# Performance work log

Hardware: AMD Instinct MI355X
Metric: run time of the kernel (lower is better)

## Reference

```python
import jax, jax.numpy as jnp
import numpy as np

N_BATCH, S, CH = 16384, 7, 30  # B*5+num_classes = 2*5+20
CO_COORD, CO_NOOBJ = 5.0, 0.5


def setup_inputs() -> dict:
    key = jax.random.key(0)
    k1, k2, k3 = jax.random.split(key, 3)
    preds = jax.random.uniform(k1, (N_BATCH, S, S, CH), dtype=jnp.float32)
    targets = jax.random.uniform(k2, (N_BATCH, S, S, CH), dtype=jnp.float32)
    obj = (jax.random.uniform(k3, (N_BATCH, S, S)) > 0.7).astype(jnp.float32)
    targets = targets.at[..., 4].set(obj * targets[..., 4] + obj * 1e-3)
    return {"preds": preds, "targets": targets}


def reference(preds, targets):
    # NOTE: faithful to the original torch code, including its bug where
    # coo_target is taken from preds (so box_target/class_target == the
    # predictions), making loc_loss and class_loss identically zero while
    # contain_loss compares pred confidence against (detached) IoU.
    N = preds.shape[0]
    P = preds.reshape(-1, CH)            # [NC, 30], NC = N*S*S
    T = targets.reshape(-1, CH)
    conf_t = T[:, 4]
    coo = (conf_t > 0).astype(preds.dtype)   # cells with object
    noo = (conf_t == 0).astype(preds.dtype)  # cells without object

    # --- no-object confidence loss (channels 4 and 9) ---
    nooobj_loss = jnp.sum(noo * ((P[:, 4] - T[:, 4]) ** 2 + (P[:, 9] - T[:, 9]) ** 2))

    # --- per-cell box matching (vectorized version of the python loop) ---
    boxes = P[:, :10].reshape(-1, 2, 5)       # [NC, 2, 5] predicted boxes
    xy = boxes[..., :2] / 14.0                # 14.0 == 2*S hardcoded upstream
    wh = boxes[..., 2:4]
    lt1 = xy - 0.5 * wh                       # [NC, 2, 2]
    rb1 = xy + 0.5 * wh
    tbox = boxes[:, 0]                        # box2 = box_target[i] == first pred box (bug)
    lt2 = tbox[:, :2] / 14.0 - 0.5 * tbox[:, 2:4]  # [NC, 2]
    rb2 = tbox[:, :2] / 14.0 + 0.5 * tbox[:, 2:4]

    ilt = jnp.maximum(lt1, lt2[:, None, :])
    irb = jnp.minimum(rb1, rb2[:, None, :])
    iwh = jnp.maximum(irb - ilt, 0.0)
    inter = iwh[..., 0] * iwh[..., 1]                    # [NC, 2]
    area1 = (rb1 - lt1)[..., 0] * (rb1 - lt1)[..., 1]    # [NC, 2]
    area2 = ((rb2 - lt2)[..., 0] * (rb2 - lt2)[..., 1])[:, None]
    iou = inter / (area1 + area2 - inter)                # [NC, 2]

    max_iou = jnp.max(iou, axis=1)                       # [NC]
    idx = jnp.argmax(iou, axis=1)                        # [NC] in {0,1}
    resp = jnp.take_along_axis(boxes, idx[:, None, None], axis=1)[:, 0]       # responsible box
    nresp = jnp.take_along_axis(boxes, (1 - idx)[:, None, None], axis=1)[:, 0]
    tgt_resp = resp  # box_target == box_pred due to the upstream bug

    # contain: pred conf vs detached IoU (original uses max_iou.data)
    contain_loss = jnp.sum(coo * (resp[:, 4] - jax.lax.stop_gradient(max_iou)) ** 2)
    # loc: identically zero given the bug, but computed faithfully
    loc_loss = (jnp.sum(coo[:, None] * (resp[:, :2] - tgt_resp[:, :2]) ** 2)
                + jnp.sum(coo[:, None] * (jnp.sqrt(resp[:, 2:4]) - jnp.sqrt(tgt_resp[:, 2:4])) ** 2))
    # not-responsible box: target conf zeroed
    not_contain_loss = jnp.sum(coo * nresp[:, 4] ** 2)
    # class loss: class_target also taken from preds (bug) -> zero
    cls = P[:, 10:]
    class_loss = jnp.sum(coo[:, None] * (cls - cls) ** 2)

    total = (CO_COORD * loc_loss + contain_loss + CO_NOOBJ * not_contain_loss
             + CO_NOOBJ * nooobj_loss + class_loss) / N
    return total
```

## Files before the change

### kernel.cpp

```cpp
#include <hip/hip_runtime.h>


#define TILE 256

__device__ __forceinline__ float cell_loss(const float p[10], float t4, float t9) {
    float coo = (t4 > 0.0f) ? 1.0f : 0.0f;
    float noo = (t4 == 0.0f) ? 1.0f : 0.0f;

    float d4 = p[4] - t4;
    float d9 = p[9] - t9;
    float noo_term = noo * (d4 * d4 + d9 * d9);

    float lt2x = p[0] / 14.0f - 0.5f * p[2];
    float lt2y = p[1] / 14.0f - 0.5f * p[3];
    float rb2x = p[0] / 14.0f + 0.5f * p[2];
    float rb2y = p[1] / 14.0f + 0.5f * p[3];
    float area2 = (rb2x - lt2x) * (rb2y - lt2y);

    float iou[2];
    #pragma unroll
    for (int b = 0; b < 2; ++b) {
        float x = p[5 * b] / 14.0f;
        float y = p[5 * b + 1] / 14.0f;
        float w = p[5 * b + 2];
        float h = p[5 * b + 3];
        float lt1x = x - 0.5f * w, lt1y = y - 0.5f * h;
        float rb1x = x + 0.5f * w, rb1y = y + 0.5f * h;
        float iltx = fmaxf(lt1x, lt2x), ilty = fmaxf(lt1y, lt2y);
        float irbx = fminf(rb1x, rb2x), irby = fminf(rb1y, rb2y);
        float iwx = fmaxf(irbx - iltx, 0.0f);
        float iwy = fmaxf(irby - ilty, 0.0f);
        float inter = iwx * iwy;
        float area1 = (rb1x - lt1x) * (rb1y - lt1y);
        iou[b] = inter / (area1 + area2 - inter);
    }

    int idx;
    float max_iou;
    if (isnan(iou[0]))      { idx = 0; max_iou = iou[0]; }
    else if (isnan(iou[1])) { idx = 1; max_iou = iou[1]; }
    else                    { idx = (iou[1] > iou[0]) ? 1 : 0;
                              max_iou = fmaxf(iou[0], iou[1]); }

    float resp4  = p[5 * idx + 4];
    float nresp4 = p[5 * (1 - idx) + 4];
    float cdiff  = resp4 - max_iou;
    return coo * (cdiff * cdiff + 0.5f * nresp4 * nresp4) + 0.5f * noo_term;
}

__global__ __launch_bounds__(256) void yolo_loss_kernel(
    const float* __restrict__ preds,
    const float* __restrict__ targets,
    float* __restrict__ partials,
    int ncells)
{
    __shared__ float4 smem4[768];
    __shared__ float  warp_sums[4];
    float2* S2 = reinterpret_cast<float2*>(smem4);
    float*  Tc = reinterpret_cast<float*>(smem4 + 640);

    const int tid = threadIdx.x;
    const long tile0 = (long)blockIdx.x * TILE;
    float contrib = 0.0f;

    if (tile0 + TILE <= ncells) {
        const float4* gp = reinterpret_cast<const float4*>(preds + tile0 * 30);
        const float4* gt = reinterpret_cast<const float4*>(targets + tile0 * 30);

        float4 pv[3];
        #pragma unroll
        for (int k = 0; k < 3; ++k) {
            int L = tid + 256 * k;
            int pair = L / 6, rr = L - pair * 6;
            int r = (rr < 3) ? rr : rr + 4;
            pv[k] = gp[pair * 15 + r];
        }
        float4 tv[2];
        #pragma unroll
        for (int k = 0; k < 2; ++k) {
            int L = tid + 256 * k;
            int pair = L / 4, rr = L & 3;
            int r = (rr < 2) ? rr + 1 : rr + 6;
            tv[k] = gt[pair * 15 + r];
        }

        #pragma unroll
        for (int k = 0; k < 3; ++k) {
            int L = tid + 256 * k;
            int pair = L / 6, rr = L - pair * 6;
            if (rr == 2) {
                S2[(pair * 5 + 2) * 2] = make_float2(pv[k].x, pv[k].y);
            } else if (rr == 3) {
                S2[(pair * 5 + 2) * 2 + 1] = make_float2(pv[k].z, pv[k].w);
            } else {
                int slot = (rr < 2) ? rr : rr - 1;
                smem4[pair * 5 + slot] = pv[k];
            }
        }
        #pragma unroll
        for (int k = 0; k < 2; ++k) {
            int L = tid + 256 * k;
            int pair = L / 4, rr = L & 3;
            float v = (rr == 0) ? tv[k].x : (rr == 1) ? tv[k].y
                    : (rr == 2) ? tv[k].z : tv[k].w;
            Tc[pair * 4 + rr] = v;
        }
        __syncthreads();

        float p[10];
        #pragma unroll
        for (int k = 0; k < 5; ++k) {
            float2 q = S2[5 * tid + k];
            p[2 * k]     = q.x;
            p[2 * k + 1] = q.y;
        }
        float t4 = Tc[2 * tid];
        float t9 = Tc[2 * tid + 1];
        contrib = cell_loss(p, t4, t9);
    } else {
        long cell = tile0 + tid;
        if (cell < ncells) {
            long base = cell * 30;
            float p[10];
            #pragma unroll
            for (int k = 0; k < 5; ++k) {
                float2 v = *reinterpret_cast<const float2*>(preds + base + 2 * k);
                p[2 * k] = v.x;
                p[2 * k + 1] = v.y;
            }
            contrib = cell_loss(p, targets[base + 4], targets[base + 9]);
        }
        __syncthreads();
    }

    #pragma unroll
    for (int off = 32; off > 0; off >>= 1)
        contrib += __shfl_down(contrib, off, 64);

    int lane = tid & 63;
    int wid  = tid >> 6;
    if (lane == 0) warp_sums[wid] = contrib;
    __syncthreads();

    if (tid == 0) {
        partials[blockIdx.x] = warp_sums[0] + warp_sums[1] + warp_sums[2] + warp_sums[3];
    }
}

__global__ __launch_bounds__(256) void yolo_reduce_kernel(
    const float* __restrict__ partials,
    float* __restrict__ out,
    int nparts)
{
    __shared__ float warp_sums[4];
    const int tid = threadIdx.x;

    float s = 0.0f;
    for (int i = tid; i < nparts; i += 256)
        s += partials[i];

    #pragma unroll
    for (int off = 32; off > 0; off >>= 1)
        s += __shfl_down(s, off, 64);

    int lane = tid & 63;
    int wid  = tid >> 6;
    if (lane == 0) warp_sums[wid] = s;
    __syncthreads();

    if (tid == 0) {
        out[0] = (warp_sums[0] + warp_sums[1] + warp_sums[2] + warp_sums[3])
                 * (1.0f / 16384.0f);
    }
}

extern "C" void kernel_launch(void* const* d_in, const int* in_sizes, int n_in,
                              void* d_out, int out_size, void* d_ws, size_t ws_size,
                              hipStream_t stream) {
    const float* preds   = (const float*)d_in[0];
    const float* targets = (const float*)d_in[1];
    float* out = (float*)d_out;
    float* partials = (float*)d_ws;

    int ncells = in_sizes[0] / 30;
    int grid = (ncells + TILE - 1) / TILE;

    yolo_loss_kernel<<<grid, 256, 0, stream>>>(preds, targets, partials, ncells);
    yolo_reduce_kernel<<<1, 256, 0, stream>>>(partials, out, grid);
}
```

Measured before the change: 37.25 us.

## Process two tiles per block, prefetching the second tile during compute of the first

```diff
diff --git a/kernel.cpp b/kernel.cpp
--- a/kernel.cpp
+++ b/kernel.cpp
@@ -2,6 +2,7 @@
 
 
 #define TILE 256
+#define NT   2
 
 __device__ __forceinline__ float cell_loss(const float p[10], float t4, float t9) {
     float coo = (t4 > 0.0f) ? 1.0f : 0.0f;
@@ -48,6 +49,60 @@
     return coo * (cdiff * cdiff + 0.5f * nresp4 * nresp4) + 0.5f * noo_term;
 }
 
+struct TileRegs { float4 pv[3]; float4 tv[2]; };
+
+__device__ __forceinline__ void issue_tile(const float* __restrict__ preds,
+                                           const float* __restrict__ targets,
+                                           long tile0, int tid, TileRegs& R) {
+    const float4* gp = reinterpret_cast<const float4*>(preds + tile0 * 30);
+    const float4* gt = reinterpret_cast<const float4*>(targets + tile0 * 30);
+    #pragma unroll
+    for (int k = 0; k < 3; ++k) {
+        int L = tid + 256 * k;
+        int pair = L / 6, rr = L - pair * 6;
+        int r = (rr < 3) ? rr : rr + 4;
+        R.pv[k] = gp[pair * 15 + r];
+    }
+    #pragma unroll
+    for (int k = 0; k < 2; ++k) {
+        int L = tid + 256 * k;
+        int pair = L / 4, rr = L & 3;
+        int r = (rr < 2) ? rr + 1 : rr + 6;
+        R.tv[k] = gt[pair * 15 + r];
+    }
+}
+
+__device__ __forceinline__ void write_tile(float4* smem4, float2* S2, float* Tc,
+                                           int tid, const TileRegs& R) {
+    #pragma unroll
+    for (int k = 0; k < 3; ++k) {
+        int L = tid + 256 * k;
+        int pair = L / 6, rr = L - pair * 6;
+        if (rr == 2)      S2[(pair * 5 + 2) * 2]     = make_float2(R.pv[k].x, R.pv[k].y);
+        else if (rr == 3) S2[(pair * 5 + 2) * 2 + 1] = make_float2(R.pv[k].z, R.pv[k].w);
+        else { int slot = (rr < 2) ? rr : rr - 1; smem4[pair * 5 + slot] = R.pv[k]; }
+    }
+    #pragma unroll
+    for (int k = 0; k < 2; ++k) {
+        int L = tid + 256 * k;
+        int pair = L / 4, rr = L & 3;
+        float v = (rr == 0) ? R.tv[k].x : (rr == 1) ? R.tv[k].y
+                : (rr == 2) ? R.tv[k].z : R.tv[k].w;
+        Tc[pair * 4 + rr] = v;
+    }
+}
+
+__device__ __forceinline__ float compute_tile(const float2* S2, const float* Tc, int tid) {
+    float p[10];
+    #pragma unroll
+    for (int k = 0; k < 5; ++k) {
+        float2 q = S2[5 * tid + k];
+        p[2 * k]     = q.x;
+        p[2 * k + 1] = q.y;
+    }
+    return cell_loss(p, Tc[2 * tid], Tc[2 * tid + 1]);
+}
+
 __global__ __launch_bounds__(256) void yolo_loss_kernel(
     const float* __restrict__ preds,
     const float* __restrict__ targets,
@@ -60,77 +115,37 @@
     float*  Tc = reinterpret_cast<float*>(smem4 + 640);
 
     const int tid = threadIdx.x;
-    const long tile0 = (long)blockIdx.x * TILE;
+    const long tA = (long)blockIdx.x * (NT * TILE);
+    const long tB = tA + TILE;
     float contrib = 0.0f;
 
-    if (tile0 + TILE <= ncells) {
-        const float4* gp = reinterpret_cast<const float4*>(preds + tile0 * 30);
-        const float4* gt = reinterpret_cast<const float4*>(targets + tile0 * 30);
-
-        float4 pv[3];
+    if (tB + TILE <= ncells) {
+        TileRegs A, B;
+        issue_tile(preds, targets, tA, tid, A);
+        write_tile(smem4, S2, Tc, tid, A);
+        __syncthreads();
+        issue_tile(preds, targets, tB, tid, B);
+        contrib = compute_tile(S2, Tc, tid);
+        __syncthreads();
+        write_tile(smem4, S2, Tc, tid, B);
+        __syncthreads();
+        contrib += compute_tile(S2, Tc, tid);
+    } else {
         #pragma unroll
-        for (int k = 0; k < 3; ++k) {
-            int L = tid + 256 * k;
-            int pair = L / 6, rr = L - pair * 6;
-            int r = (rr < 3) ? rr : rr + 4;
-            pv[k] = gp[pair * 15 + r];
-        }
-        float4 tv[2];
-        #pragma unroll
-        for (int k = 0; k < 2; ++k) {
-            int L = tid + 256 * k;
-            int pair = L / 4, rr = L & 3;
-            int r = (rr < 2) ? rr + 1 : rr + 6;
-            tv[k] = gt[pair * 15 + r];
-        }
-
-        #pragma unroll
-        for (int k = 0; k < 3; ++k) {
-            int L = tid + 256 * k;
-            int pair = L / 6, rr = L - pair * 6;
-            if (rr == 2) {
-                S2[(pair * 5 + 2) * 2] = make_float2(pv[k].x, pv[k].y);
-            } else if (rr == 3) {
-                S2[(pair * 5 + 2) * 2 + 1] = make_float2(pv[k].z, pv[k].w);
-            } else {
-                int slot = (rr < 2) ? rr : rr - 1;
-                smem4[pair * 5 + slot] = pv[k];
+        for (int t = 0; t < NT; ++t) {
+            long cell = tA + (long)t * TILE + tid;
+            if (cell < ncells) {
+                long base = cell * 30;
+                float p[10];
+                #pragma unroll
+                for (int k = 0; k < 5; ++k) {
+                    float2 v = *reinterpret_cast<const float2*>(preds + base + 2 * k);
+                    p[2 * k] = v.x;
+                    p[2 * k + 1] = v.y;
+                }
+                contrib += cell_loss(p, targets[base + 4], targets[base + 9]);
             }
         }
-        #pragma unroll
-        for (int k = 0; k < 2; ++k) {
-            int L = tid + 256 * k;
-            int pair = L / 4, rr = L & 3;
-            float v = (rr == 0) ? tv[k].x : (rr == 1) ? tv[k].y
-                    : (rr == 2) ? tv[k].z : tv[k].w;
-            Tc[pair * 4 + rr] = v;
-        }
-        __syncthreads();
-
-        float p[10];
-        #pragma unroll
-        for (int k = 0; k < 5; ++k) {
-            float2 q = S2[5 * tid + k];
-            p[2 * k]     = q.x;
-            p[2 * k + 1] = q.y;
-        }
-        float t4 = Tc[2 * tid];
-        float t9 = Tc[2 * tid + 1];
-        contrib = cell_loss(p, t4, t9);
-    } else {
-        long cell = tile0 + tid;
-        if (cell < ncells) {
-            long base = cell * 30;
-            float p[10];
-            #pragma unroll
-            for (int k = 0; k < 5; ++k) {
-                float2 v = *reinterpret_cast<const float2*>(preds + base + 2 * k);
-                p[2 * k] = v.x;
-                p[2 * k + 1] = v.y;
-            }
-            contrib = cell_loss(p, targets[base + 4], targets[base + 9]);
-        }
-        __syncthreads();
     }
 
     #pragma unroll
@@ -183,7 +198,7 @@
     float* partials = (float*)d_ws;
 
     int ncells = in_sizes[0] / 30;
-    int grid = (ncells + TILE - 1) / TILE;
+    int grid = (ncells + NT * TILE - 1) / (NT * TILE);
 
     yolo_loss_kernel<<<grid, 256, 0, stream>>>(preds, targets, partials, ncells);
     yolo_reduce_kernel<<<1, 256, 0, stream>>>(partials, out, grid);
```

After: 36.56 us, median of 2. No clear change (-1.8%).
